# Optimization experiments

Measured on AMD Instinct MI355X. Metric: run time of the kernel, lower is better.

The kernel has to match this reference:

```python
import jax, jax.numpy as jnp
import numpy as np

B, N, DIM = 2, 2048, 512
H, DH = 8, 64
INNER = H * DH
SCALE = DH ** -0.5


def setup_inputs() -> dict:
    key = jax.random.key(0)
    ks = jax.random.split(key, 8)
    s = 0.02
    return {
        "nodes": jax.random.normal(ks[0], (B, N, DIM), dtype=jnp.float32),
        "edge_mask": jax.random.bernoulli(ks[1], 0.9, (B, N, N)),
        "wq": jax.random.normal(ks[2], (DIM, INNER), dtype=jnp.float32) * s,
        "bq": jnp.zeros((INNER,), dtype=jnp.float32),
        "wkv": jax.random.normal(ks[3], (DIM, 2 * INNER), dtype=jnp.float32) * s,
        "bkv": jnp.zeros((2 * INNER,), dtype=jnp.float32),
        "wo": jax.random.normal(ks[4], (INNER, DIM), dtype=jnp.float32) * s,
        "bo": jnp.zeros((DIM,), dtype=jnp.float32),
    }


def reference(nodes, edge_mask, wq, bq, wkv, bkv, wo, bo):
    b, n, _ = nodes.shape
    q = nodes @ wq + bq                      # [b, n, h*dh]
    kv = nodes @ wkv + bkv                   # [b, n, 2*h*dh]
    k, v = jnp.split(kv, 2, axis=-1)
    # split heads -> [b, h, n, dh]
    split = lambda t: t.reshape(b, n, H, DH).transpose(0, 2, 1, 3)
    q, k, v = split(q), split(k), split(v)
    sim = jnp.einsum('bhid,bhjd->bhij', q, k) * SCALE
    max_neg = -jnp.finfo(sim.dtype).max
    sim = jnp.where(edge_mask[:, None, :, :], sim, max_neg)
    attn = jax.nn.softmax(sim, axis=-1)
    out = jnp.einsum('bhij,bhjd->bhid', attn, v)      # [b, h, n, dh]
    out = out.transpose(0, 2, 1, 3).reshape(b, n, INNER)
    return out @ wo + bo
```

## Files before the change

### kernel.cpp

```cpp
#include <hip/hip_runtime.h>
#include <cstdint>
#include <cstddef>

#define DEVI __device__ __forceinline__

typedef __bf16 bf16x8 __attribute__((ext_vector_type(8)));
typedef float floatx4 __attribute__((ext_vector_type(4)));
typedef unsigned short us4v __attribute__((ext_vector_type(4)));
typedef unsigned short us8 __attribute__((ext_vector_type(8)));
typedef short short4v __attribute__((ext_vector_type(4)));

static_assert(sizeof(bf16x8) == 16, "bf16x8 must be 16B");
static_assert(sizeof(us8) == 16, "us8 must be 16B");


#if __has_builtin(__builtin_amdgcn_cvt_pk_bf16_f32)
DEVI unsigned short f2bf(float f) {
  typedef __bf16 bf16x2 __attribute__((ext_vector_type(2)));
  union { bf16x2 v; unsigned short u[2]; } c;
  c.v = __builtin_amdgcn_cvt_pk_bf16_f32(f, 0.f);
  return c.u[0];
}
#else
DEVI unsigned short f2bf(float f) {
  unsigned int u = __float_as_uint(f);
  u += 0x7fffu + ((u >> 16) & 1u);
  return (unsigned short)(u >> 16);
}
#endif

DEVI float exp2c(float x) {
#if __has_builtin(__builtin_amdgcn_exp2f)
  return __builtin_amdgcn_exp2f(x);
#else
  return exp2f(x);
#endif
}

DEVI bf16x8 ld8(const unsigned short* p) { return *(const bf16x8*)p; }

typedef const __attribute__((address_space(1))) void* gas_ptr;
typedef __attribute__((address_space(3))) void* las_ptr;

DEVI void gld16(const void* g, void* l) {
  __builtin_amdgcn_global_load_lds((gas_ptr)g, (las_ptr)l, 16, 0, 0);
}

#define WAIT_LGKM0() __builtin_amdgcn_s_waitcnt(0xc07f)

__global__ __launch_bounds__(256) void pack_k(const void* m, unsigned int* pm) {
  __shared__ int mode;
  const unsigned int* md = (const unsigned int*)m;
  unsigned int probe = md[threadIdx.x];
  bool odd = (probe > 1u && probe != 0x3f800000u);
  if (threadIdx.x == 0) mode = 0;
  __syncthreads();
  if (odd) atomicOr(&mode, 1);
  __syncthreads();
  int byteMode = mode;

  int t = blockIdx.x * 256 + threadIdx.x;
  int lane = threadIdx.x & 63;
  unsigned int n;
  if (byteMode) {
    unsigned int x = md[t];
    n = ((x & 0xffu) ? 1u : 0u) | ((x & 0xff00u) ? 2u : 0u) |
        ((x & 0xff0000u) ? 4u : 0u) | ((x >> 24) ? 8u : 0u);
  } else {
    uint4 v = ((const uint4*)m)[t];
    n = (v.x ? 1u : 0u) | (v.y ? 2u : 0u) | (v.z ? 4u : 0u) | (v.w ? 8u : 0u);
  }
  unsigned int w = n << ((lane & 7) * 4);
  w |= __shfl_xor(w, 1);
  w |= __shfl_xor(w, 2);
  w |= __shfl_xor(w, 4);
  if ((lane & 7) == 0) pm[t >> 3] = w;
}

__global__ void cvt_x_k(const float* __restrict__ x, unsigned short* __restrict__ xb) {
  int i = blockIdx.x * 256 + threadIdx.x;
  float4 v = ((const float4*)x)[i];
  us4v o;
  o[0] = f2bf(v.x); o[1] = f2bf(v.y); o[2] = f2bf(v.z); o[3] = f2bf(v.w);
  *(us4v*)(xb + (size_t)i * 4) = o;
}

__global__ __launch_bounds__(256) void transpose_all_k(
    const float* __restrict__ wq, const float* __restrict__ wkv,
    const float* __restrict__ wo,
    unsigned short* __restrict__ WQKVT, unsigned short* __restrict__ WOT) {
  const float* src; unsigned short* dst; int C, c0;
  int z = blockIdx.z;
  if (z == 0)      { if (blockIdx.x >= 8) return; src = wq;  dst = WQKVT; C = 512;  c0 = 0; }
  else if (z == 1) { src = wkv; dst = WQKVT; C = 1024; c0 = 512; }
  else             { if (blockIdx.x >= 8) return; src = wo;  dst = WOT;  C = 512;  c0 = 0; }
  __shared__ unsigned short t2[64 * 64];
  const int t = threadIdx.x;
  const int ct = blockIdx.x * 64, rt = blockIdx.y * 64;
  for (int p = 0; p < 4; p++) {
    int kl = p * 16 + (t >> 4);
    int cc = (t & 15) * 4;
    float4 v = *(const float4*)&src[(size_t)(rt + kl) * C + ct + cc];
    float f[4] = {v.x, v.y, v.z, v.w};
    for (int i = 0; i < 4; i++) {
      int c = cc + i;
      t2[c * 64 + (kl ^ (c & 56))] = f2bf(f[i]);
    }
  }
  __syncthreads();
  for (int p = 0; p < 2; p++) {
    int c = p * 32 + (t >> 3);
    int kc = (t & 7) * 8;
    us8 v = *(const us8*)&t2[c * 64 + (kc ^ (c & 56))];
    *(us8*)&dst[(size_t)(c0 + ct + c) * 512 + rt + kc] = v;
  }
}

__global__ __launch_bounds__(256) void gemm_qkv_k(
    const unsigned short* __restrict__ A,
    const unsigned short* __restrict__ Bt,
    const float* __restrict__ bq, const float* __restrict__ bkv,
    unsigned short* __restrict__ Qo, unsigned short* __restrict__ Ko,
    unsigned short* __restrict__ VTo) {
  __shared__ unsigned short smem[8192];
  unsigned short* sA = smem;
  unsigned short* sB = smem + 2048;
  const int tid = threadIdx.x;
  const int wave = tid >> 6, lane = tid & 63, quad = lane >> 4, l16 = lane & 15;
  const int wm = wave >> 1, wn = wave & 1;
  const int bm = blockIdx.x, bn = blockIdx.y;
  floatx4 acc[2][4] = {};
  const int arow = lane >> 2;
  const int ag = lane & 3;
  for (int kt = 0; kt < 16; kt++) {
    __syncthreads();
    {
      int rowA = wave * 16 + arow;
      int gA = ag ^ (rowA & 3);
      gld16(&A[(size_t)(bm * 64 + rowA) * 512 + kt * 32 + gA * 8], &sA[(wave * 16) * 32]);
      for (int p = 0; p < 2; p++) {
        int rowB = p * 64 + wave * 16 + arow;
        int gB = ag ^ (rowB & 3);
        gld16(&Bt[(size_t)(bn * 128 + rowB) * 512 + kt * 32 + gB * 8],
              &sB[(p * 64 + wave * 16) * 32]);
      }
    }
    __syncthreads();
    bf16x8 aF[2], bF[4];
    int swz = (quad ^ (l16 & 3)) * 8;
    for (int i = 0; i < 2; i++) aF[i] = ld8(&sA[(wm * 32 + i * 16 + l16) * 32 + swz]);
    for (int j = 0; j < 4; j++) bF[j] = ld8(&sB[(wn * 64 + j * 16 + l16) * 32 + swz]);
    for (int i = 0; i < 2; i++)
      for (int j = 0; j < 4; j++)
        acc[i][j] = __builtin_amdgcn_mfma_f32_16x16x32_bf16(aF[i], bF[j], acc[i][j], 0, 0, 0);
  }

  const int sec = bn * 2 + wn;
  float bias[4];
  float scale = 1.0f;
  if (sec < 8) {
    for (int j = 0; j < 4; j++) bias[j] = bq[sec * 64 + j * 16 + l16];
    scale = 0.18033688011112042f;
  } else {
    for (int j = 0; j < 4; j++) bias[j] = bkv[(sec - 8) * 64 + j * 16 + l16];
  }
  const int gr0 = bm * 64 + wm * 32;
  const int b = gr0 >> 11, n0 = gr0 & 2047;
  unsigned short* pw = smem + wave * 2048;
  __syncthreads();
  if (sec < 16) {
    for (int i = 0; i < 2; i++)
      for (int j = 0; j < 4; j++) {
        int cg = j * 2 + (l16 >> 3), ci = l16 & 7;
        for (int r = 0; r < 4; r++) {
          int row = i * 16 + quad * 4 + r;
          pw[row * 64 + ((cg ^ (row & 7)) * 8) + ci] = f2bf((acc[i][j][r] + bias[j]) * scale);
        }
      }
    WAIT_LGKM0();
    unsigned short* dst = (sec < 8) ? Qo + ((size_t)(b * 8 + sec) * 2048 + n0) * 64
                                    : Ko + ((size_t)(b * 8 + sec - 8) * 2048 + n0) * 64;
    for (int p = 0; p < 4; p++) {
      int row = p * 8 + (lane >> 3);
      int c8 = lane & 7;
      us8 v = *(const us8*)&pw[row * 64 + ((c8 ^ (row & 7)) * 8)];
      *(us8*)&dst[(size_t)row * 64 + c8 * 8] = v;
    }
  } else {
    for (int i = 0; i < 2; i++)
      for (int j = 0; j < 4; j++) {
        int d = j * 16 + l16;
        int ng = i * 2 + (quad >> 1), n7 = (quad & 1) * 4;
        for (int r = 0; r < 4; r++)
          pw[d * 32 + ((ng ^ (d & 3)) * 8) + n7 + r] = f2bf(acc[i][j][r] + bias[j]);
      }
    WAIT_LGKM0();
    unsigned short* dst = VTo + (size_t)(b * 8 + sec - 16) * 64 * 2048 + n0;
    for (int p = 0; p < 4; p++) {
      int d = p * 16 + (lane >> 2);
      int c4 = lane & 3;
      us8 v = *(const us8*)&pw[d * 32 + ((c4 ^ (d & 3)) * 8)];
      *(us8*)&dst[(size_t)d * 2048 + c4 * 8] = v;
    }
  }
}

__global__ __launch_bounds__(128, 4) void attn_k(
    const unsigned short* __restrict__ Q,
    const unsigned short* __restrict__ K,
    const unsigned short* __restrict__ Vt,
    const unsigned int* __restrict__ pm,
    unsigned short* __restrict__ AO) {
  __shared__ unsigned short kT[4096];
  __shared__ unsigned short vT[4096];
  __shared__ unsigned short pA[2][1024];
  const int tid = threadIdx.x;
  const int wave = tid >> 6, lane = tid & 63, quad = lane >> 4, l16 = lane & 15;
  const int qt = blockIdx.x, bh = blockIdx.y, b = bh >> 3, h = bh & 7;
  const int q0 = qt * 32 + wave * 16;
  const unsigned short* Qb = Q + (size_t)bh * 2048 * 64;
  const unsigned short* Kb = K + (size_t)bh * 2048 * 64;
  const unsigned short* Vb = Vt + (size_t)bh * 64 * 2048;
  const unsigned int* pmB = pm + (size_t)b * 2048 * 64;

  bf16x8 qF0 = ld8(&Qb[(size_t)(q0 + l16) * 64 + quad * 8]);
  bf16x8 qF1 = ld8(&Qb[(size_t)(q0 + l16) * 64 + 32 + quad * 8]);

  floatx4 oacc[4] = {};
  float lsum = 0.f;

  const int sw0 = (quad ^ (l16 & 7)) * 8;
  const int sw1 = ((4 + quad) ^ (l16 & 7)) * 8;
  const int srow = wave * 8 + (lane >> 3);
  const int sg = lane & 7;
  const int vg = ((quad >> 1) ^ (l16 & 7)) * 8;

  for (int it = 0; it < 32; ++it) {
    const int k0 = it * 64;
    __syncthreads();
    for (int p = 0; p < 4; p++) {
      int row = p * 16 + srow;
      int g = sg ^ (row & 7);
      gld16(&Kb[(size_t)(k0 + row) * 64 + g * 8], &kT[(p * 16 + wave * 8) * 64]);
      gld16(&Vb[(size_t)row * 2048 + k0 + g * 8], &vT[(p * 16 + wave * 8) * 64]);
    }
    uint2 mw = *(const uint2*)&pmB[(size_t)(q0 + l16) * 64 + it * 2];
    __syncthreads();

    floatx4 st[4];
    for (int kb = 0; kb < 4; kb++) {
      bf16x8 kf0 = ld8(&kT[(kb * 16 + l16) * 64 + sw0]);
      bf16x8 kf1 = ld8(&kT[(kb * 16 + l16) * 64 + sw1]);
      floatx4 z = {0.f, 0.f, 0.f, 0.f};
      z = __builtin_amdgcn_mfma_f32_16x16x32_bf16(kf0, qF0, z, 0, 0, 0);
      st[kb] = __builtin_amdgcn_mfma_f32_16x16x32_bf16(kf1, qF1, z, 0, 0, 0);
    }

    union { short4v s4; unsigned short u[4]; unsigned int d[2]; } pf[4];
    for (int kb = 0; kb < 4; kb++) {
      unsigned int w = (kb < 2) ? mw.x : mw.y;
      int base = (kb & 1) * 16 + quad * 4;
      for (int r = 0; r < 4; r++) {
        float e = exp2c(st[kb][r]);
        e = ((w >> (base + r)) & 1u) ? e : 0.f;
        lsum += e;
        pf[kb].u[r] = f2bf(e);
      }
    }

#if __has_builtin(__builtin_amdgcn_mfma_f32_16x16x16bf16_1k)
    for (int kb = 0; kb < 4; kb++) {
      int off = ((kb * 2 + (quad >> 1)) ^ (l16 & 7)) * 8 + (quad & 1) * 4;
      for (int db = 0; db < 4; db++) {
        short4v a = *(const short4v*)&vT[(db * 16 + l16) * 64 + off];
        oacc[db] = __builtin_amdgcn_mfma_f32_16x16x16bf16_1k(a, pf[kb].s4, oacc[db], 0, 0, 0);
      }
    }
#else
    for (int kb = 0; kb < 4; kb++) {
      union { bf16x8 v; unsigned int d[4]; } bf;
      if (quad & 1) { bf.d[0] = 0; bf.d[1] = 0; bf.d[2] = pf[kb].d[0]; bf.d[3] = pf[kb].d[1]; }
      else          { bf.d[0] = pf[kb].d[0]; bf.d[1] = pf[kb].d[1]; bf.d[2] = 0; bf.d[3] = 0; }
      int off = ((kb * 2 + (quad >> 1)) ^ (l16 & 7)) * 8;
      for (int db = 0; db < 4; db++) {
        bf16x8 a = ld8(&vT[(db * 16 + l16) * 64 + off]);
        oacc[db] = __builtin_amdgcn_mfma_f32_16x16x32_bf16(a, bf.v, oacc[db], 0, 0, 0);
      }
    }
#endif
  }

  lsum += __shfl_xor(lsum, 16);
  lsum += __shfl_xor(lsum, 32);
  float inv = 1.0f / lsum;

  unsigned short* pw = pA[wave];
  for (int db = 0; db < 4; db++) {
    int cg = db * 2 + (quad >> 1);
    for (int r = 0; r < 4; r++) {
      int col = db * 16 + quad * 4 + r;
      pw[l16 * 64 + ((cg ^ (l16 & 7)) * 8) + (col & 7)] = f2bf(oacc[db][r] * inv);
    }
  }
  WAIT_LGKM0();
  for (int p = 0; p < 2; p++) {
    int row = p * 8 + (lane >> 3);
    int c8 = lane & 7;
    us8 v = *(const us8*)&pw[row * 64 + ((c8 ^ (row & 7)) * 8)];
    *(us8*)&AO[((size_t)b * 2048 + q0 + row) * 512 + h * 64 + c8 * 8] = v;
  }
  (void)vg;
}

__global__ __launch_bounds__(256) void gemm_out_k(
    const unsigned short* __restrict__ A,
    const unsigned short* __restrict__ Bt,
    const float* __restrict__ bo, float* __restrict__ out) {
  __shared__ unsigned short smem[6144];
  unsigned short* sA = smem;
  unsigned short* sB = smem + 2048;
  const int tid = threadIdx.x;
  const int wave = tid >> 6, lane = tid & 63, quad = lane >> 4, l16 = lane & 15;
  const int wm = wave >> 1, wn = wave & 1;
  const int bm = blockIdx.x, bn = blockIdx.y;
  floatx4 acc[2][4] = {};
  const int arow = lane >> 2;
  const int ag = lane & 3;
  for (int kt = 0; kt < 16; kt++) {
    __syncthreads();
    {
      int rowA = wave * 16 + arow;
      int gA = ag ^ (rowA & 3);
      gld16(&A[(size_t)(bm * 64 + rowA) * 512 + kt * 32 + gA * 8], &sA[(wave * 16) * 32]);
      for (int p = 0; p < 2; p++) {
        int rowB = p * 64 + wave * 16 + arow;
        int gB = ag ^ (rowB & 3);
        gld16(&Bt[(size_t)(bn * 128 + rowB) * 512 + kt * 32 + gB * 8],
              &sB[(p * 64 + wave * 16) * 32]);
      }
    }
    __syncthreads();
    bf16x8 aF[2], bF[4];
    int swz = (quad ^ (l16 & 3)) * 8;
    for (int i = 0; i < 2; i++) aF[i] = ld8(&sA[(wm * 32 + i * 16 + l16) * 32 + swz]);
    for (int j = 0; j < 4; j++) bF[j] = ld8(&sB[(wn * 64 + j * 16 + l16) * 32 + swz]);
    for (int i = 0; i < 2; i++)
      for (int j = 0; j < 4; j++)
        acc[i][j] = __builtin_amdgcn_mfma_f32_16x16x32_bf16(aF[i], bF[j], acc[i][j], 0, 0, 0);
  }
  for (int i = 0; i < 2; i++)
    for (int j = 0; j < 4; j++) {
      int gc = bn * 128 + wn * 64 + j * 16 + l16;
      float bb = bo[gc];
      for (int r = 0; r < 4; r++) {
        int gr = bm * 64 + wm * 32 + i * 16 + quad * 4 + r;
        out[(size_t)gr * 512 + gc] = acc[i][j][r] + bb;
      }
    }
}

extern "C" void kernel_launch(void* const* d_in, const int* in_sizes, int n_in,
                              void* d_out, int out_size, void* d_ws, size_t ws_size,
                              hipStream_t stream) {
  const float* nodes = (const float*)d_in[0];
  const void*  mask  = d_in[1];
  const float* wq    = (const float*)d_in[2];
  const float* bq    = (const float*)d_in[3];
  const float* wkv   = (const float*)d_in[4];
  const float* bkv   = (const float*)d_in[5];
  const float* wo    = (const float*)d_in[6];
  const float* bo    = (const float*)d_in[7];
  float* out = (float*)d_out;

  char* ws = (char*)d_ws;
  unsigned short* XB    = (unsigned short*)(ws + 0);
  unsigned short* WQKVT = (unsigned short*)(ws + 4194304);
  unsigned short* WOT   = (unsigned short*)(ws + 5767168);
  unsigned short* Qm    = (unsigned short*)(ws + 6291456);
  unsigned short* Km    = (unsigned short*)(ws + 10485760);
  unsigned short* VTm   = (unsigned short*)(ws + 18874368);
  unsigned short* AOm   = (unsigned short*)(ws + 23068672);
  unsigned int*   PM    = (unsigned int*)(ws + 27262976);

  pack_k<<<8192, 256, 0, stream>>>(mask, PM);
  cvt_x_k<<<2048, 256, 0, stream>>>(nodes, XB);
  transpose_all_k<<<dim3(16, 8, 3), 256, 0, stream>>>(wq, wkv, wo, WQKVT, WOT);
  gemm_qkv_k<<<dim3(64, 12), 256, 0, stream>>>(XB, WQKVT, bq, bkv, Qm, Km, VTm);
  attn_k<<<dim3(64, 16), 128, 0, stream>>>(Qm, Km, VTm, PM, AOm);
  gemm_out_k<<<dim3(64, 4), 256, 0, stream>>>(AOm, WOT, bo, out);
}
```

Measured before the change: 169.6 us.

## Restructure attention into split-K waves with 64-query tiles and fuse prep kernels

The three preprocessing kernels (mask packing, input bf16 conversion, weight transposes) are merged into one launch dispatched by block index, saving launch overhead. The attention kernel now uses 256-thread blocks that each cover 64 queries. Each wave processes its own 64-key slice with 16x16x32 MFMAs, so K/V fragments are reused across four query blocks. Partial outputs and row sums are then reduced across the waves through shared memory. The V^T epilogue in the QKV GEMM is also changed to vectorized LDS stores. In exchange the attention kernel holds more registers and shared memory per block and adds a cross-wave reduction.

```diff
diff --git a/kernel.cpp b/kernel.cpp
--- a/kernel.cpp
+++ b/kernel.cpp
@@ -8,7 +8,6 @@
 typedef float floatx4 __attribute__((ext_vector_type(4)));
 typedef unsigned short us4v __attribute__((ext_vector_type(4)));
 typedef unsigned short us8 __attribute__((ext_vector_type(8)));
-typedef short short4v __attribute__((ext_vector_type(4)));
 
 static_assert(sizeof(bf16x8) == 16, "bf16x8 must be 16B");
 static_assert(sizeof(us8) == 16, "us8 must be 16B");
@@ -48,71 +47,72 @@
 
 #define WAIT_LGKM0() __builtin_amdgcn_s_waitcnt(0xc07f)
 
-__global__ __launch_bounds__(256) void pack_k(const void* m, unsigned int* pm) {
-  __shared__ int mode;
-  const unsigned int* md = (const unsigned int*)m;
-  unsigned int probe = md[threadIdx.x];
-  bool odd = (probe > 1u && probe != 0x3f800000u);
-  if (threadIdx.x == 0) mode = 0;
-  __syncthreads();
-  if (odd) atomicOr(&mode, 1);
-  __syncthreads();
-  int byteMode = mode;
-
-  int t = blockIdx.x * 256 + threadIdx.x;
-  int lane = threadIdx.x & 63;
-  unsigned int n;
-  if (byteMode) {
-    unsigned int x = md[t];
-    n = ((x & 0xffu) ? 1u : 0u) | ((x & 0xff00u) ? 2u : 0u) |
-        ((x & 0xff0000u) ? 4u : 0u) | ((x >> 24) ? 8u : 0u);
-  } else {
-    uint4 v = ((const uint4*)m)[t];
-    n = (v.x ? 1u : 0u) | (v.y ? 2u : 0u) | (v.z ? 4u : 0u) | (v.w ? 8u : 0u);
-  }
-  unsigned int w = n << ((lane & 7) * 4);
-  w |= __shfl_xor(w, 1);
-  w |= __shfl_xor(w, 2);
-  w |= __shfl_xor(w, 4);
-  if ((lane & 7) == 0) pm[t >> 3] = w;
-}
-
-__global__ void cvt_x_k(const float* __restrict__ x, unsigned short* __restrict__ xb) {
-  int i = blockIdx.x * 256 + threadIdx.x;
-  float4 v = ((const float4*)x)[i];
-  us4v o;
-  o[0] = f2bf(v.x); o[1] = f2bf(v.y); o[2] = f2bf(v.z); o[3] = f2bf(v.w);
-  *(us4v*)(xb + (size_t)i * 4) = o;
-}
-
-__global__ __launch_bounds__(256) void transpose_all_k(
+__global__ __launch_bounds__(256) void prep_k(
+    const float* __restrict__ nodes, const void* __restrict__ mask,
     const float* __restrict__ wq, const float* __restrict__ wkv,
     const float* __restrict__ wo,
-    unsigned short* __restrict__ WQKVT, unsigned short* __restrict__ WOT) {
-  const float* src; unsigned short* dst; int C, c0;
-  int z = blockIdx.z;
-  if (z == 0)      { if (blockIdx.x >= 8) return; src = wq;  dst = WQKVT; C = 512;  c0 = 0; }
-  else if (z == 1) { src = wkv; dst = WQKVT; C = 1024; c0 = 512; }
-  else             { if (blockIdx.x >= 8) return; src = wo;  dst = WOT;  C = 512;  c0 = 0; }
-  __shared__ unsigned short t2[64 * 64];
-  const int t = threadIdx.x;
-  const int ct = blockIdx.x * 64, rt = blockIdx.y * 64;
-  for (int p = 0; p < 4; p++) {
-    int kl = p * 16 + (t >> 4);
-    int cc = (t & 15) * 4;
-    float4 v = *(const float4*)&src[(size_t)(rt + kl) * C + ct + cc];
-    float f[4] = {v.x, v.y, v.z, v.w};
-    for (int i = 0; i < 4; i++) {
-      int c = cc + i;
-      t2[c * 64 + (kl ^ (c & 56))] = f2bf(f[i]);
-    }
-  }
-  __syncthreads();
-  for (int p = 0; p < 2; p++) {
-    int c = p * 32 + (t >> 3);
-    int kc = (t & 7) * 8;
-    us8 v = *(const us8*)&t2[c * 64 + (kc ^ (c & 56))];
-    *(us8*)&dst[(size_t)(c0 + ct + c) * 512 + rt + kc] = v;
+    unsigned short* __restrict__ XB, unsigned short* __restrict__ WQKVT,
+    unsigned short* __restrict__ WOT, unsigned int* __restrict__ pm) {
+  int bid = blockIdx.x;
+  if (bid < 8192) {
+    __shared__ int mode;
+    const unsigned int* md = (const unsigned int*)mask;
+    unsigned int probe = md[threadIdx.x];
+    bool odd = (probe > 1u && probe != 0x3f800000u);
+    if (threadIdx.x == 0) mode = 0;
+    __syncthreads();
+    if (odd) atomicOr(&mode, 1);
+    __syncthreads();
+    int byteMode = mode;
+    int t = bid * 256 + threadIdx.x;
+    int lane = threadIdx.x & 63;
+    unsigned int n;
+    if (byteMode) {
+      unsigned int x = md[t];
+      n = ((x & 0xffu) ? 1u : 0u) | ((x & 0xff00u) ? 2u : 0u) |
+          ((x & 0xff0000u) ? 4u : 0u) | ((x >> 24) ? 8u : 0u);
+    } else {
+      uint4 v = ((const uint4*)mask)[t];
+      n = (v.x ? 1u : 0u) | (v.y ? 2u : 0u) | (v.z ? 4u : 0u) | (v.w ? 8u : 0u);
+    }
+    unsigned int w = n << ((lane & 7) * 4);
+    w |= __shfl_xor(w, 1);
+    w |= __shfl_xor(w, 2);
+    w |= __shfl_xor(w, 4);
+    if ((lane & 7) == 0) pm[t >> 3] = w;
+  } else if (bid < 10240) {
+    int i = (bid - 8192) * 256 + threadIdx.x;
+    float4 v = ((const float4*)nodes)[i];
+    us4v o;
+    o[0] = f2bf(v.x); o[1] = f2bf(v.y); o[2] = f2bf(v.z); o[3] = f2bf(v.w);
+    *(us4v*)(XB + (size_t)i * 4) = o;
+  } else {
+    int tb = bid - 10240;
+    int x = tb & 15, y = (tb >> 4) & 7, z = tb >> 7;
+    const float* src; unsigned short* dst; int C, c0;
+    if (z == 0)      { if (x >= 8) return; src = wq;  dst = WQKVT; C = 512;  c0 = 0; }
+    else if (z == 1) { src = wkv; dst = WQKVT; C = 1024; c0 = 512; }
+    else             { if (x >= 8) return; src = wo;  dst = WOT;  C = 512;  c0 = 0; }
+    __shared__ unsigned short t2[64 * 64];
+    const int t = threadIdx.x;
+    const int ct = x * 64, rt = y * 64;
+    for (int p = 0; p < 4; p++) {
+      int kl = p * 16 + (t >> 4);
+      int cc = (t & 15) * 4;
+      float4 v = *(const float4*)&src[(size_t)(rt + kl) * C + ct + cc];
+      float f[4] = {v.x, v.y, v.z, v.w};
+      for (int i = 0; i < 4; i++) {
+        int c = cc + i;
+        t2[c * 64 + (kl ^ (c & 56))] = f2bf(f[i]);
+      }
+    }
+    __syncthreads();
+    for (int p = 0; p < 2; p++) {
+      int c = p * 32 + (t >> 3);
+      int kc = (t & 7) * 8;
+      us8 v = *(const us8*)&t2[c * 64 + (kc ^ (c & 56))];
+      *(us8*)&dst[(size_t)(c0 + ct + c) * 512 + rt + kc] = v;
+    }
   }
 }
 
@@ -190,9 +190,9 @@
     for (int i = 0; i < 2; i++)
       for (int j = 0; j < 4; j++) {
         int d = j * 16 + l16;
-        int ng = i * 2 + (quad >> 1), n7 = (quad & 1) * 4;
-        for (int r = 0; r < 4; r++)
-          pw[d * 32 + ((ng ^ (d & 3)) * 8) + n7 + r] = f2bf(acc[i][j][r] + bias[j]);
+        us4v t;
+        for (int r = 0; r < 4; r++) t[r] = f2bf(acc[i][j][r] + bias[j]);
+        *(us4v*)&pw[d * 32 + ((quad ^ (d & 3)) * 8) + i * 4] = t;
       }
     WAIT_LGKM0();
     unsigned short* dst = VTo + (size_t)(b * 8 + sec - 16) * 64 * 2048 + n0;
@@ -205,111 +205,118 @@
   }
 }
 
-__global__ __launch_bounds__(128, 4) void attn_k(
+__global__ __launch_bounds__(256, 2) void attn_k(
     const unsigned short* __restrict__ Q,
     const unsigned short* __restrict__ K,
     const unsigned short* __restrict__ Vt,
     const unsigned int* __restrict__ pm,
     unsigned short* __restrict__ AO) {
-  __shared__ unsigned short kT[4096];
-  __shared__ unsigned short vT[4096];
-  __shared__ unsigned short pA[2][1024];
+  __shared__ unsigned short kT[4][4096];
+  __shared__ unsigned short vT[4][4096];
+  __shared__ float lsumB[4][64];
   const int tid = threadIdx.x;
   const int wave = tid >> 6, lane = tid & 63, quad = lane >> 4, l16 = lane & 15;
-  const int qt = blockIdx.x, bh = blockIdx.y, b = bh >> 3, h = bh & 7;
-  const int q0 = qt * 32 + wave * 16;
+  const int bh = blockIdx.x, qt = blockIdx.y, b = bh >> 3, h = bh & 7;
+  const int q0 = qt * 64;
   const unsigned short* Qb = Q + (size_t)bh * 2048 * 64;
   const unsigned short* Kb = K + (size_t)bh * 2048 * 64;
   const unsigned short* Vb = Vt + (size_t)bh * 64 * 2048;
   const unsigned int* pmB = pm + (size_t)b * 2048 * 64;
 
-  bf16x8 qF0 = ld8(&Qb[(size_t)(q0 + l16) * 64 + quad * 8]);
-  bf16x8 qF1 = ld8(&Qb[(size_t)(q0 + l16) * 64 + 32 + quad * 8]);
-
-  floatx4 oacc[4] = {};
-  float lsum = 0.f;
-
-  const int sw0 = (quad ^ (l16 & 7)) * 8;
-  const int sw1 = ((4 + quad) ^ (l16 & 7)) * 8;
-  const int srow = wave * 8 + (lane >> 3);
-  const int sg = lane & 7;
-  const int vg = ((quad >> 1) ^ (l16 & 7)) * 8;
-
-  for (int it = 0; it < 32; ++it) {
-    const int k0 = it * 64;
-    __syncthreads();
-    for (int p = 0; p < 4; p++) {
-      int row = p * 16 + srow;
-      int g = sg ^ (row & 7);
-      gld16(&Kb[(size_t)(k0 + row) * 64 + g * 8], &kT[(p * 16 + wave * 8) * 64]);
-      gld16(&Vb[(size_t)row * 2048 + k0 + g * 8], &vT[(p * 16 + wave * 8) * 64]);
-    }
-    uint2 mw = *(const uint2*)&pmB[(size_t)(q0 + l16) * 64 + it * 2];
-    __syncthreads();
-
-    floatx4 st[4];
-    for (int kb = 0; kb < 4; kb++) {
-      bf16x8 kf0 = ld8(&kT[(kb * 16 + l16) * 64 + sw0]);
-      bf16x8 kf1 = ld8(&kT[(kb * 16 + l16) * 64 + sw1]);
-      floatx4 z = {0.f, 0.f, 0.f, 0.f};
-      z = __builtin_amdgcn_mfma_f32_16x16x32_bf16(kf0, qF0, z, 0, 0, 0);
-      st[kb] = __builtin_amdgcn_mfma_f32_16x16x32_bf16(kf1, qF1, z, 0, 0, 0);
-    }
-
-    union { short4v s4; unsigned short u[4]; unsigned int d[2]; } pf[4];
-    for (int kb = 0; kb < 4; kb++) {
-      unsigned int w = (kb < 2) ? mw.x : mw.y;
-      int base = (kb & 1) * 16 + quad * 4;
-      for (int r = 0; r < 4; r++) {
-        float e = exp2c(st[kb][r]);
-        e = ((w >> (base + r)) & 1u) ? e : 0.f;
-        lsum += e;
-        pf[kb].u[r] = f2bf(e);
-      }
-    }
-
-#if __has_builtin(__builtin_amdgcn_mfma_f32_16x16x16bf16_1k)
-    for (int kb = 0; kb < 4; kb++) {
-      int off = ((kb * 2 + (quad >> 1)) ^ (l16 & 7)) * 8 + (quad & 1) * 4;
+  bf16x8 qF[4][2];
+  for (int qb = 0; qb < 4; qb++) {
+    qF[qb][0] = ld8(&Qb[(size_t)(q0 + qb * 16 + l16) * 64 + quad * 8]);
+    qF[qb][1] = ld8(&Qb[(size_t)(q0 + qb * 16 + l16) * 64 + 32 + quad * 8]);
+  }
+
+  floatx4 oacc[4][4] = {};
+  float lsum[4] = {0.f, 0.f, 0.f, 0.f};
+
+  const int srow = lane >> 3;
+  const int gK = (lane & 7) ^ srow;
+  const int rsw0 = quad ^ (l16 & 7);
+  const int rsw1 = (4 + quad) ^ (l16 & 7);
+
+  for (int it = 0; it < 8; ++it) {
+    const int k0w = it * 256 + wave * 64;
+    for (int p = 0; p < 8; p++) {
+      gld16(&Kb[(size_t)(k0w + p * 8 + srow) * 64 + gK * 8], &kT[wave][p * 512]);
+      gld16(&Vb[(size_t)(p * 8 + srow) * 2048 + k0w + gK * 8], &vT[wave][p * 512]);
+    }
+    uint2 mw[4];
+    for (int qb = 0; qb < 4; qb++)
+      mw[qb] = *(const uint2*)&pmB[(size_t)(q0 + qb * 16 + l16) * 64 + it * 8 + wave * 2];
+    __syncthreads();
+
+    for (int c = 0; c < 2; c++) {
+      floatx4 st[4][2];
+      for (int k2 = 0; k2 < 2; k2++) {
+        const unsigned short* kr = &kT[wave][((c * 2 + k2) * 16 + l16) * 64];
+        bf16x8 kf0 = ld8(kr + rsw0 * 8);
+        bf16x8 kf1 = ld8(kr + rsw1 * 8);
+        for (int qb = 0; qb < 4; qb++) {
+          floatx4 z = {0.f, 0.f, 0.f, 0.f};
+          z = __builtin_amdgcn_mfma_f32_16x16x32_bf16(kf0, qF[qb][0], z, 0, 0, 0);
+          st[qb][k2] = __builtin_amdgcn_mfma_f32_16x16x32_bf16(kf1, qF[qb][1], z, 0, 0, 0);
+        }
+      }
+      union uB { bf16x8 v; unsigned short u[8]; } pf[4];
+      for (int qb = 0; qb < 4; qb++) {
+        unsigned int w = c ? mw[qb].y : mw[qb].x;
+        for (int k2 = 0; k2 < 2; k2++) {
+          int base = k2 * 16 + quad * 4;
+          for (int r = 0; r < 4; r++) {
+            float e = exp2c(st[qb][k2][r]);
+            e = ((w >> (base + r)) & 1u) ? e : 0.f;
+            lsum[qb] += e;
+            pf[qb].u[k2 * 4 + r] = f2bf(e);
+          }
+        }
+      }
       for (int db = 0; db < 4; db++) {
-        short4v a = *(const short4v*)&vT[(db * 16 + l16) * 64 + off];
-        oacc[db] = __builtin_amdgcn_mfma_f32_16x16x16bf16_1k(a, pf[kb].s4, oacc[db], 0, 0, 0);
-      }
-    }
-#else
-    for (int kb = 0; kb < 4; kb++) {
-      union { bf16x8 v; unsigned int d[4]; } bf;
-      if (quad & 1) { bf.d[0] = 0; bf.d[1] = 0; bf.d[2] = pf[kb].d[0]; bf.d[3] = pf[kb].d[1]; }
-      else          { bf.d[0] = pf[kb].d[0]; bf.d[1] = pf[kb].d[1]; bf.d[2] = 0; bf.d[3] = 0; }
-      int off = ((kb * 2 + (quad >> 1)) ^ (l16 & 7)) * 8;
-      for (int db = 0; db < 4; db++) {
-        bf16x8 a = ld8(&vT[(db * 16 + l16) * 64 + off]);
-        oacc[db] = __builtin_amdgcn_mfma_f32_16x16x32_bf16(a, bf.v, oacc[db], 0, 0, 0);
-      }
-    }
-#endif
-  }
-
-  lsum += __shfl_xor(lsum, 16);
-  lsum += __shfl_xor(lsum, 32);
-  float inv = 1.0f / lsum;
-
-  unsigned short* pw = pA[wave];
-  for (int db = 0; db < 4; db++) {
-    int cg = db * 2 + (quad >> 1);
-    for (int r = 0; r < 4; r++) {
-      int col = db * 16 + quad * 4 + r;
-      pw[l16 * 64 + ((cg ^ (l16 & 7)) * 8) + (col & 7)] = f2bf(oacc[db][r] * inv);
-    }
-  }
-  WAIT_LGKM0();
-  for (int p = 0; p < 2; p++) {
-    int row = p * 8 + (lane >> 3);
-    int c8 = lane & 7;
-    us8 v = *(const us8*)&pw[row * 64 + ((c8 ^ (row & 7)) * 8)];
-    *(us8*)&AO[((size_t)b * 2048 + q0 + row) * 512 + h * 64 + c8 * 8] = v;
-  }
-  (void)vg;
+        int row = db * 16 + l16;
+        bf16x8 va = ld8(&vT[wave][row * 64 + (((c * 4 + quad) ^ (row & 7)) * 8)]);
+        for (int qb = 0; qb < 4; qb++)
+          oacc[db][qb] =
+              __builtin_amdgcn_mfma_f32_16x16x32_bf16(va, pf[qb].v, oacc[db][qb], 0, 0, 0);
+      }
+    }
+    __syncthreads();
+  }
+
+  for (int qb = 0; qb < 4; qb++) {
+    lsum[qb] += __shfl_xor(lsum[qb], 16);
+    lsum[qb] += __shfl_xor(lsum[qb], 32);
+  }
+  lsumB[wave][quad * 16 + l16] = lsum[quad];
+
+  float* pO = (float*)&kT[0][0];
+  float* myR = pO + wave * 4096;
+  for (int db = 0; db < 4; db++)
+    for (int qb = 0; qb < 4; qb++) {
+      int q = qb * 16 + l16;
+      *(floatx4*)&myR[q * 64 + (((db * 4 + quad) ^ l16) & 15) * 4] = oacc[db][qb];
+    }
+  __syncthreads();
+  {
+    int q = tid >> 2, dblk = tid & 3;
+    float inv = 1.0f / (lsumB[0][q] + lsumB[1][q] + lsumB[2][q] + lsumB[3][q]);
+    float o[16];
+    for (int i = 0; i < 4; i++) {
+      int dg = dblk * 4 + i;
+      int off = q * 64 + ((dg ^ q) & 15) * 4;
+      floatx4 s = *(floatx4*)&pO[off];
+      s += *(floatx4*)&pO[4096 + off];
+      s += *(floatx4*)&pO[8192 + off];
+      s += *(floatx4*)&pO[12288 + off];
+      for (int r = 0; r < 4; r++) o[i * 4 + r] = s[r] * inv;
+    }
+    us8 v0, v1;
+    for (int i = 0; i < 8; i++) { v0[i] = f2bf(o[i]); v1[i] = f2bf(o[8 + i]); }
+    unsigned short* dst = &AO[((size_t)b * 2048 + q0 + q) * 512 + h * 64 + dblk * 16];
+    *(us8*)dst = v0;
+    *(us8*)(dst + 8) = v1;
+  }
 }
 
 __global__ __launch_bounds__(256) void gemm_out_k(
@@ -382,10 +389,8 @@
   unsigned short* AOm   = (unsigned short*)(ws + 23068672);
   unsigned int*   PM    = (unsigned int*)(ws + 27262976);
 
-  pack_k<<<8192, 256, 0, stream>>>(mask, PM);
-  cvt_x_k<<<2048, 256, 0, stream>>>(nodes, XB);
-  transpose_all_k<<<dim3(16, 8, 3), 256, 0, stream>>>(wq, wkv, wo, WQKVT, WOT);
+  prep_k<<<10624, 256, 0, stream>>>(nodes, mask, wq, wkv, wo, XB, WQKVT, WOT, PM);
   gemm_qkv_k<<<dim3(64, 12), 256, 0, stream>>>(XB, WQKVT, bq, bkv, Qm, Km, VTm);
-  attn_k<<<dim3(64, 16), 128, 0, stream>>>(Qm, Km, VTm, PM, AOm);
+  attn_k<<<dim3(16, 32), 256, 0, stream>>>(Qm, Km, VTm, PM, AOm);
   gemm_out_k<<<dim3(64, 4), 256, 0, stream>>>(AOm, WOT, bo, out);
 }
```

After: 153.5 us. -9.5%, faster.
